# Kernel optimization log

Hardware: AMD Instinct MI355X
Metric: run time of the kernel (lower is better)

## Reference

```python
import jax, jax.numpy as jnp
import numpy as np

N_NODES = 50000
N_EDGES = 800000
IN_FEATS = 64
HIDDEN = 32
HEADS = 8
NEG_SLOPE = 0.2


def gat_conv(x, W, a_l, a_r, b, src, dst, num_nodes):
    """DGL-style GATConv. x:[N,in], W:[in,H,O], a_l/a_r/b:[H,O]. Returns [N,H,O]."""
    feat = jnp.einsum('ni,iho->nho', x, W)              # [N,H,O]
    el = jnp.sum(feat * a_l, axis=-1)                   # [N,H]
    er = jnp.sum(feat * a_r, axis=-1)                   # [N,H]
    e = jax.nn.leaky_relu(el[src] + er[dst], NEG_SLOPE) # [E,H]
    # segment softmax over incoming edges of each dst node
    m = jax.ops.segment_max(e, dst, num_segments=num_nodes)   # [N,H]
    ex = jnp.exp(e - m[dst])                                   # [E,H]
    s = jax.ops.segment_sum(ex, dst, num_segments=num_nodes)   # [N,H]
    alpha = ex / s[dst]                                        # [E,H]
    out = jax.ops.segment_sum(feat[src] * alpha[:, :, None], dst,
                              num_segments=num_nodes)          # [N,H,O]
    return out + b


def setup_inputs() -> dict:
    key = jax.random.key(0)
    ks = jax.random.split(key, 12)
    g1 = 1.0 / np.sqrt(IN_FEATS)
    g2 = 1.0 / np.sqrt(HIDDEN * HEADS)
    return {
        'features': jax.random.normal(ks[0], (N_NODES, IN_FEATS), jnp.float32),
        'src': jax.random.randint(ks[1], (N_EDGES,), 0, N_NODES, jnp.int32),
        'dst': jax.random.randint(ks[2], (N_EDGES,), 0, N_NODES, jnp.int32),
        'edge_types': jax.random.randint(ks[3], (N_EDGES,), 0, 4, jnp.int32),
        'W1': jax.random.normal(ks[4], (IN_FEATS, HEADS, HIDDEN), jnp.float32) * g1,
        'al1': jax.random.normal(ks[5], (HEADS, HIDDEN), jnp.float32) * g1,
        'ar1': jax.random.normal(ks[6], (HEADS, HIDDEN), jnp.float32) * g1,
        'b1': jnp.zeros((HEADS, HIDDEN), jnp.float32),
        'W2': jax.random.normal(ks[7], (HIDDEN * HEADS, 1, 1), jnp.float32) * g2,
        'al2': jax.random.normal(ks[8], (1, 1), jnp.float32) * g2,
        'ar2': jax.random.normal(ks[9], (1, 1), jnp.float32) * g2,
        'b2': jnp.zeros((1, 1), jnp.float32),
    }


def reference(features, src, dst, edge_types, W1, al1, ar1, b1, W2, al2, ar2, b2):
    h = gat_conv(features, W1, al1, ar1, b1, src, dst, N_NODES)  # [N,H,O]
    h = jax.nn.relu(h.reshape(h.shape[0], -1))                   # [N,H*O]
    h = gat_conv(h, W2, al2, ar2, b2, src, dst, N_NODES)         # [N,1,1]
    h = jnp.squeeze(h, axis=1)                                   # [N,1]
    return jax.nn.sigmoid(h)
```

## Files before the change

kernel.cpp:

```cpp
#include <hip/hip_runtime.h>

#define N_NODES 50000
#define N_EDGES 800000
#define FEAT_BLOCKS 3125
#define CAP 64

typedef unsigned int uint32;
typedef unsigned short ushort16;
typedef unsigned char uchar8;
typedef short bf8v __attribute__((ext_vector_type(8)));
typedef float f32x4 __attribute__((ext_vector_type(4)));

__device__ __forceinline__ ushort16 f2bf(float f) {
  uint32 u = __float_as_uint(f);
  u += 0x7fffu + ((u >> 16) & 1u);
  return (ushort16)(u >> 16);
}

__global__ __launch_bounds__(256) void k_init(const float* __restrict__ W1,
    ushort16* __restrict__ w1t, int4* __restrict__ deg4) {
  int b = blockIdx.x, t = threadIdx.x;
  if (b < 64) {
    int col = b * 4 + (t >> 6), k = t & 63;
    w1t[col * 64 + k] = f2bf(W1[k * 256 + col]);
  } else {
    int i = (b - 64) * 256 + t;
    if (i < 12500) deg4[i] = make_int4(0, 0, 0, 0);
  }
}

__global__ __launch_bounds__(256) void k_build_feat(const float* __restrict__ x,
    const ushort16* __restrict__ w1t, const float* __restrict__ al1,
    const float* __restrict__ ar1, uchar8* __restrict__ feat8,
    float* __restrict__ el1, float* __restrict__ er1,
    const int* __restrict__ src, const int* __restrict__ dst,
    int* __restrict__ deg, unsigned short* __restrict__ esrc16) {
  int t = threadIdx.x;
  int q = blockIdx.x / 5, r = blockIdx.x % 5;
  if (r == 4) {
    int e0 = q * 1024 + t;
#pragma unroll
    for (int j = 0; j < 4; ++j) {
      int e = e0 + j * 256;
      if (e < N_EDGES) {
        int d = dst[e];
        int sV = src[e];
        int p = atomicAdd(&deg[d], 1);
        if (p < CAP) esrc16[d * CAP + p] = (unsigned short)sV;
      }
    }
    return;
  }
  int fidx = q * 4 + r;
  if (fidx >= FEAT_BLOCKS) return;
  int w = t >> 6, lane = t & 63;
  int quad = lane >> 4, m = lane & 15;
  int n0 = fidx * 16;
  const float* xr = x + (n0 + m) * 64 + quad * 8;
  float4 xa = *(const float4*)(xr);
  float4 xbv = *(const float4*)(xr + 4);
  float4 xc = *(const float4*)(xr + 32);
  float4 xd = *(const float4*)(xr + 36);
  bf8v a0, a1;
  a0[0] = (short)f2bf(xa.x); a0[1] = (short)f2bf(xa.y);
  a0[2] = (short)f2bf(xa.z); a0[3] = (short)f2bf(xa.w);
  a0[4] = (short)f2bf(xbv.x); a0[5] = (short)f2bf(xbv.y);
  a0[6] = (short)f2bf(xbv.z); a0[7] = (short)f2bf(xbv.w);
  a1[0] = (short)f2bf(xc.x); a1[1] = (short)f2bf(xc.y);
  a1[2] = (short)f2bf(xc.z); a1[3] = (short)f2bf(xc.w);
  a1[4] = (short)f2bf(xd.x); a1[5] = (short)f2bf(xd.y);
  a1[6] = (short)f2bf(xd.z); a1[7] = (short)f2bf(xd.w);
  float pl0[4] = {0.f, 0.f, 0.f, 0.f}, pr0[4] = {0.f, 0.f, 0.f, 0.f};
  float pl1[4] = {0.f, 0.f, 0.f, 0.f}, pr1[4] = {0.f, 0.f, 0.f, 0.f};
#pragma unroll
  for (int nt = 0; nt < 4; ++nt) {
    int colg = w * 64 + nt * 16 + m;
    const bf8v* bw = (const bf8v*)(w1t + colg * 64 + quad * 8);
    bf8v b0 = bw[0];
    bf8v b1 = bw[4];
    f32x4 acc = {0.f, 0.f, 0.f, 0.f};
    acc = __builtin_amdgcn_mfma_f32_16x16x32_bf16(a0, b0, acc, 0, 0, 0);
    acc = __builtin_amdgcn_mfma_f32_16x16x32_bf16(a1, b1, acc, 0, 0, 0);
    float al = al1[colg], ar = ar1[colg];
#pragma unroll
    for (int i = 0; i < 4; ++i) {
      uint32 pb = (uint32)__builtin_amdgcn_cvt_pk_fp8_f32(acc[i], acc[i], 0, 0);
      feat8[(size_t)(n0 + quad * 4 + i) * 256 + colg] = (uchar8)(pb & 0xffu);
      if (nt < 2) { pl0[i] += acc[i] * al; pr0[i] += acc[i] * ar; }
      else        { pl1[i] += acc[i] * al; pr1[i] += acc[i] * ar; }
    }
  }
#pragma unroll
  for (int off = 1; off < 16; off <<= 1) {
#pragma unroll
    for (int i = 0; i < 4; ++i) {
      pl0[i] += __shfl_xor(pl0[i], off, 64);
      pr0[i] += __shfl_xor(pr0[i], off, 64);
      pl1[i] += __shfl_xor(pl1[i], off, 64);
      pr1[i] += __shfl_xor(pr1[i], off, 64);
    }
  }
  if (m == 0) {
#pragma unroll
    for (int i = 0; i < 4; ++i) {
      int n = n0 + quad * 4 + i;
      el1[n * 8 + 2 * w] = pl0[i];
      er1[n * 8 + 2 * w] = pr0[i];
      el1[n * 8 + 2 * w + 1] = pl1[i];
      er1[n * 8 + 2 * w + 1] = pr1[i];
    }
  }
}

#define ACC8F8(u, ex)                                                    \
  {                                                                      \
    auto p0 = __builtin_amdgcn_cvt_pk_f32_fp8((u).x, 0);                 \
    auto p1 = __builtin_amdgcn_cvt_pk_f32_fp8((u).x, 1);                 \
    auto p2 = __builtin_amdgcn_cvt_pk_f32_fp8((u).y, 0);                 \
    auto p3 = __builtin_amdgcn_cvt_pk_f32_fp8((u).y, 1);                 \
    acc[0] += p0[0] * (ex); acc[1] += p0[1] * (ex);                      \
    acc[2] += p1[0] * (ex); acc[3] += p1[1] * (ex);                      \
    acc[4] += p2[0] * (ex); acc[5] += p2[1] * (ex);                      \
    acc[6] += p3[0] * (ex); acc[7] += p3[1] * (ex);                      \
  }

__global__ __launch_bounds__(256) void k_agg1(const int* __restrict__ deg,
    const unsigned short* __restrict__ esrc16, const uint2* __restrict__ featv,
    const float* __restrict__ el1, const float* __restrict__ er1,
    const float* __restrict__ b1, const float* __restrict__ W2,
    float* __restrict__ feat2) {
  int t = threadIdx.x, nl = t >> 5, lt = t & 31;
  int n = blockIdx.x * 8 + nl;
  int h = lt >> 2;
  int begin = n * CAP;
  int d = deg[n]; d = d > CAP ? CAP : d;
  int end = begin + d;
  float er_h = er1[n * 8 + h];
  float acc[8] = {0.f, 0.f, 0.f, 0.f, 0.f, 0.f, 0.f, 0.f};
  float s = 0.f;
  int e = begin;
  for (; e + 8 <= end; e += 8) {
    uint4 sv = *(const uint4*)(esrc16 + e);
    int sn[8] = {(int)(sv.x & 0xffffu), (int)(sv.x >> 16),
                 (int)(sv.y & 0xffffu), (int)(sv.y >> 16),
                 (int)(sv.z & 0xffffu), (int)(sv.z >> 16),
                 (int)(sv.w & 0xffffu), (int)(sv.w >> 16)};
    uint2 u[8];
    float ex[8];
#pragma unroll
    for (int j = 0; j < 8; ++j) u[j] = featv[sn[j] * 32 + lt];
#pragma unroll
    for (int j = 0; j < 8; ++j) {
      float v = el1[sn[j] * 8 + h] + er_h;
      v = v > 0.f ? v : 0.2f * v;
      ex[j] = __expf(v);
      s += ex[j];
    }
#pragma unroll
    for (int j = 0; j < 8; ++j) ACC8F8(u[j], ex[j]);
  }
  for (; e + 4 <= end; e += 4) {
    int sn[4];
    uint2 u[4];
    float ex[4];
#pragma unroll
    for (int j = 0; j < 4; ++j) sn[j] = (int)esrc16[e + j];
#pragma unroll
    for (int j = 0; j < 4; ++j) u[j] = featv[sn[j] * 32 + lt];
#pragma unroll
    for (int j = 0; j < 4; ++j) {
      float v = el1[sn[j] * 8 + h] + er_h;
      v = v > 0.f ? v : 0.2f * v;
      ex[j] = __expf(v);
      s += ex[j];
    }
#pragma unroll
    for (int j = 0; j < 4; ++j) ACC8F8(u[j], ex[j]);
  }
  for (; e < end; ++e) {
    int s0 = (int)esrc16[e];
    uint2 u0 = featv[s0 * 32 + lt];
    float v0 = el1[s0 * 8 + h] + er_h;
    v0 = v0 > 0.f ? v0 : 0.2f * v0;
    float ex0 = __expf(v0);
    s += ex0;
    ACC8F8(u0, ex0);
  }
  float inv = (d > 0) ? 1.f / s : 0.f;
  int o = lt * 8;
  float4 bb0 = *(const float4*)(b1 + o), bb1 = *(const float4*)(b1 + o + 4);
  float4 ww0 = *(const float4*)(W2 + o), ww1 = *(const float4*)(W2 + o + 4);
  float r = fmaxf(acc[0] * inv + bb0.x, 0.f) * ww0.x
          + fmaxf(acc[1] * inv + bb0.y, 0.f) * ww0.y
          + fmaxf(acc[2] * inv + bb0.z, 0.f) * ww0.z
          + fmaxf(acc[3] * inv + bb0.w, 0.f) * ww0.w
          + fmaxf(acc[4] * inv + bb1.x, 0.f) * ww1.x
          + fmaxf(acc[5] * inv + bb1.y, 0.f) * ww1.y
          + fmaxf(acc[6] * inv + bb1.z, 0.f) * ww1.z
          + fmaxf(acc[7] * inv + bb1.w, 0.f) * ww1.w;
  __shared__ float red[256];
  red[t] = r;
  __syncthreads();
  for (int off = 16; off > 0; off >>= 1) {
    if (lt < off) red[t] += red[t + off];
    __syncthreads();
  }
  if (lt == 0) feat2[n] = red[t];
}

__global__ __launch_bounds__(256) void k_layer2(const int* __restrict__ deg,
    const unsigned short* __restrict__ esrc16, const float* __restrict__ feat2,
    const float* __restrict__ al2, const float* __restrict__ ar2,
    const float* __restrict__ b2, float* __restrict__ out) {
  int t = threadIdx.x, g = t >> 4, lt = t & 15;
  int n = blockIdx.x * 16 + g;
  int begin = n * CAP;
  int d = deg[n]; d = d > CAP ? CAP : d;
  int end = begin + d;
  float a2 = al2[0];
  float er_n = feat2[n] * ar2[0];
  float num = 0.f, s = 0.f;
  for (int e = begin + lt; e < end; e += 16) {
    int sN = (int)esrc16[e];
    float f = feat2[sN];
    float v = f * a2 + er_n;
    v = v > 0.f ? v : 0.2f * v;
    float ex = __expf(v);
    num += f * ex;
    s += ex;
  }
#pragma unroll
  for (int off = 8; off > 0; off >>= 1) {
    num += __shfl_down(num, off, 16);
    s += __shfl_down(s, off, 16);
  }
  if (lt == 0) {
    float val = (d > 0) ? num / s : 0.f;
    out[n] = 1.f / (1.f + __expf(-(val + b2[0])));
  }
}

extern "C" void kernel_launch(void* const* d_in, const int* in_sizes, int n_in,
                              void* d_out, int out_size, void* d_ws, size_t ws_size,
                              hipStream_t stream) {
  const float* x   = (const float*)d_in[0];
  const int* src   = (const int*)d_in[1];
  const int* dst   = (const int*)d_in[2];
  const float* W1  = (const float*)d_in[4];
  const float* al1 = (const float*)d_in[5];
  const float* ar1 = (const float*)d_in[6];
  const float* b1  = (const float*)d_in[7];
  const float* W2  = (const float*)d_in[8];
  const float* al2 = (const float*)d_in[9];
  const float* ar2 = (const float*)d_in[10];
  const float* b2  = (const float*)d_in[11];

  float* ws    = (float*)d_ws;
  float* el1   = ws;
  float* er1   = ws + 400000;
  float* feat2 = ws + 800000;
  int* deg     = (int*)ws + 850000;
  unsigned short* esrc16 = (unsigned short*)((int*)ws + 900000);
  ushort16* w1t  = (ushort16*)((int*)ws + 2500000);
  uchar8* feat8  = (uchar8*)((int*)ws + 2508192);

  k_init<<<64 + 49, 256, 0, stream>>>(W1, w1t, (int4*)deg);
  k_build_feat<<<3910, 256, 0, stream>>>(x, w1t, al1, ar1, feat8, el1, er1,
                                         src, dst, deg, esrc16);
  k_agg1<<<N_NODES / 8, 256, 0, stream>>>(deg, esrc16, (const uint2*)feat8,
                                          el1, er1, b1, W2, feat2);
  k_layer2<<<N_NODES / 16, 256, 0, stream>>>(deg, esrc16, feat2, al2, ar2, b2,
                                             (float*)d_out);
}
```

Measured before the change: 173.1 us.

## Fuse all four kernels into one persistent kernel with grid barriers

New measurement: 586.9 us. 239% more time.

```diff
diff --git a/kernel.cpp b/kernel.cpp
--- a/kernel.cpp
+++ b/kernel.cpp
@@ -2,8 +2,12 @@
 
 #define N_NODES 50000
 #define N_EDGES 800000
-#define FEAT_BLOCKS 3125
+#define FEAT_ITEMS 3125
+#define SCAT_ITEMS 782
+#define AGG_ITEMS 6250
+#define L2_ITEMS 3125
 #define CAP 64
+#define NBLK 1024
 
 typedef unsigned int uint32;
 typedef unsigned short ushort16;
@@ -17,99 +21,22 @@
   return (ushort16)(u >> 16);
 }
 
-__global__ __launch_bounds__(256) void k_init(const float* __restrict__ W1,
-    ushort16* __restrict__ w1t, int4* __restrict__ deg4) {
-  int b = blockIdx.x, t = threadIdx.x;
-  if (b < 64) {
-    int col = b * 4 + (t >> 6), k = t & 63;
-    w1t[col * 64 + k] = f2bf(W1[k * 256 + col]);
-  } else {
-    int i = (b - 64) * 256 + t;
-    if (i < 12500) deg4[i] = make_int4(0, 0, 0, 0);
-  }
-}
-
-__global__ __launch_bounds__(256) void k_build_feat(const float* __restrict__ x,
-    const ushort16* __restrict__ w1t, const float* __restrict__ al1,
-    const float* __restrict__ ar1, uchar8* __restrict__ feat8,
-    float* __restrict__ el1, float* __restrict__ er1,
-    const int* __restrict__ src, const int* __restrict__ dst,
-    int* __restrict__ deg, unsigned short* __restrict__ esrc16) {
-  int t = threadIdx.x;
-  int q = blockIdx.x / 5, r = blockIdx.x % 5;
-  if (r == 4) {
-    int e0 = q * 1024 + t;
-#pragma unroll
-    for (int j = 0; j < 4; ++j) {
-      int e = e0 + j * 256;
-      if (e < N_EDGES) {
-        int d = dst[e];
-        int sV = src[e];
-        int p = atomicAdd(&deg[d], 1);
-        if (p < CAP) esrc16[d * CAP + p] = (unsigned short)sV;
-      }
-    }
-    return;
-  }
-  int fidx = q * 4 + r;
-  if (fidx >= FEAT_BLOCKS) return;
-  int w = t >> 6, lane = t & 63;
-  int quad = lane >> 4, m = lane & 15;
-  int n0 = fidx * 16;
-  const float* xr = x + (n0 + m) * 64 + quad * 8;
-  float4 xa = *(const float4*)(xr);
-  float4 xbv = *(const float4*)(xr + 4);
-  float4 xc = *(const float4*)(xr + 32);
-  float4 xd = *(const float4*)(xr + 36);
-  bf8v a0, a1;
-  a0[0] = (short)f2bf(xa.x); a0[1] = (short)f2bf(xa.y);
-  a0[2] = (short)f2bf(xa.z); a0[3] = (short)f2bf(xa.w);
-  a0[4] = (short)f2bf(xbv.x); a0[5] = (short)f2bf(xbv.y);
-  a0[6] = (short)f2bf(xbv.z); a0[7] = (short)f2bf(xbv.w);
-  a1[0] = (short)f2bf(xc.x); a1[1] = (short)f2bf(xc.y);
-  a1[2] = (short)f2bf(xc.z); a1[3] = (short)f2bf(xc.w);
-  a1[4] = (short)f2bf(xd.x); a1[5] = (short)f2bf(xd.y);
-  a1[6] = (short)f2bf(xd.z); a1[7] = (short)f2bf(xd.w);
-  float pl0[4] = {0.f, 0.f, 0.f, 0.f}, pr0[4] = {0.f, 0.f, 0.f, 0.f};
-  float pl1[4] = {0.f, 0.f, 0.f, 0.f}, pr1[4] = {0.f, 0.f, 0.f, 0.f};
-#pragma unroll
-  for (int nt = 0; nt < 4; ++nt) {
-    int colg = w * 64 + nt * 16 + m;
-    const bf8v* bw = (const bf8v*)(w1t + colg * 64 + quad * 8);
-    bf8v b0 = bw[0];
-    bf8v b1 = bw[4];
-    f32x4 acc = {0.f, 0.f, 0.f, 0.f};
-    acc = __builtin_amdgcn_mfma_f32_16x16x32_bf16(a0, b0, acc, 0, 0, 0);
-    acc = __builtin_amdgcn_mfma_f32_16x16x32_bf16(a1, b1, acc, 0, 0, 0);
-    float al = al1[colg], ar = ar1[colg];
-#pragma unroll
-    for (int i = 0; i < 4; ++i) {
-      uint32 pb = (uint32)__builtin_amdgcn_cvt_pk_fp8_f32(acc[i], acc[i], 0, 0);
-      feat8[(size_t)(n0 + quad * 4 + i) * 256 + colg] = (uchar8)(pb & 0xffu);
-      if (nt < 2) { pl0[i] += acc[i] * al; pr0[i] += acc[i] * ar; }
-      else        { pl1[i] += acc[i] * al; pr1[i] += acc[i] * ar; }
-    }
-  }
-#pragma unroll
-  for (int off = 1; off < 16; off <<= 1) {
-#pragma unroll
-    for (int i = 0; i < 4; ++i) {
-      pl0[i] += __shfl_xor(pl0[i], off, 64);
-      pr0[i] += __shfl_xor(pr0[i], off, 64);
-      pl1[i] += __shfl_xor(pl1[i], off, 64);
-      pr1[i] += __shfl_xor(pr1[i], off, 64);
-    }
-  }
-  if (m == 0) {
-#pragma unroll
-    for (int i = 0; i < 4; ++i) {
-      int n = n0 + quad * 4 + i;
-      el1[n * 8 + 2 * w] = pl0[i];
-      er1[n * 8 + 2 * w] = pr0[i];
-      el1[n * 8 + 2 * w + 1] = pl1[i];
-      er1[n * 8 + 2 * w + 1] = pr1[i];
-    }
-  }
+__device__ __forceinline__ void gbar(int* cnt, int* gen) {
+  __syncthreads();
+  if (threadIdx.x == 0) {
+    int g = __hip_atomic_load(gen, __ATOMIC_RELAXED, __HIP_MEMORY_SCOPE_AGENT);
+    __threadfence();
+    int a = __hip_atomic_fetch_add(cnt, 1, __ATOMIC_ACQ_REL, __HIP_MEMORY_SCOPE_AGENT);
+    if (a == NBLK - 1) {
+      __hip_atomic_store(cnt, 0, __ATOMIC_RELAXED, __HIP_MEMORY_SCOPE_AGENT);
+      __hip_atomic_fetch_add(gen, 1, __ATOMIC_RELEASE, __HIP_MEMORY_SCOPE_AGENT);
+    } else {
+      while (__hip_atomic_load(gen, __ATOMIC_RELAXED, __HIP_MEMORY_SCOPE_AGENT) == g)
+        __builtin_amdgcn_s_sleep(1);
+    }
+    __threadfence();
+  }
+  __syncthreads();
 }
 
 #define ACC8F8(u, ex)                                                    \
@@ -124,119 +51,197 @@
     acc[6] += p3[0] * (ex); acc[7] += p3[1] * (ex);                      \
   }
 
-__global__ __launch_bounds__(256) void k_agg1(const int* __restrict__ deg,
-    const unsigned short* __restrict__ esrc16, const uint2* __restrict__ featv,
-    const float* __restrict__ el1, const float* __restrict__ er1,
-    const float* __restrict__ b1, const float* __restrict__ W2,
-    float* __restrict__ feat2) {
-  int t = threadIdx.x, nl = t >> 5, lt = t & 31;
-  int n = blockIdx.x * 8 + nl;
-  int h = lt >> 2;
-  int begin = n * CAP;
-  int d = deg[n]; d = d > CAP ? CAP : d;
-  int end = begin + d;
-  float er_h = er1[n * 8 + h];
-  float acc[8] = {0.f, 0.f, 0.f, 0.f, 0.f, 0.f, 0.f, 0.f};
-  float s = 0.f;
-  int e = begin;
-  for (; e + 8 <= end; e += 8) {
-    uint4 sv = *(const uint4*)(esrc16 + e);
-    int sn[8] = {(int)(sv.x & 0xffffu), (int)(sv.x >> 16),
-                 (int)(sv.y & 0xffffu), (int)(sv.y >> 16),
-                 (int)(sv.z & 0xffffu), (int)(sv.z >> 16),
-                 (int)(sv.w & 0xffffu), (int)(sv.w >> 16)};
-    uint2 u[8];
-    float ex[8];
-#pragma unroll
-    for (int j = 0; j < 8; ++j) u[j] = featv[sn[j] * 32 + lt];
-#pragma unroll
-    for (int j = 0; j < 8; ++j) {
-      float v = el1[sn[j] * 8 + h] + er_h;
+__global__ __launch_bounds__(256, 4) void k_fused(const float* __restrict__ x,
+    const float* __restrict__ W1, const float* __restrict__ al1,
+    const float* __restrict__ ar1, const float* __restrict__ b1,
+    const float* __restrict__ W2, const float* __restrict__ al2,
+    const float* __restrict__ ar2, const float* __restrict__ b2,
+    const int* __restrict__ src, const int* __restrict__ dst,
+    float* __restrict__ el1, float* __restrict__ er1, float* __restrict__ feat2,
+    int* __restrict__ deg, unsigned short* __restrict__ esrc16,
+    ushort16* __restrict__ w1t, uchar8* __restrict__ feat8,
+    int* __restrict__ bar_cnt, int* __restrict__ bar_gen,
+    float* __restrict__ out) {
+  int t = threadIdx.x;
+  __shared__ float red[256];
+
+  for (int item = blockIdx.x; item < 113; item += NBLK) {
+    if (item < 64) {
+      int col = item * 4 + (t >> 6), k = t & 63;
+      w1t[col * 64 + k] = f2bf(W1[k * 256 + col]);
+    } else {
+      int i = (item - 64) * 256 + t;
+      if (i < 12500) ((int4*)deg)[i] = make_int4(0, 0, 0, 0);
+    }
+  }
+  gbar(bar_cnt, bar_gen);
+
+  for (int item = blockIdx.x; item < FEAT_ITEMS + SCAT_ITEMS; item += NBLK) {
+    if (item >= FEAT_ITEMS) {
+      int e0 = (item - FEAT_ITEMS) * 1024 + t;
+#pragma unroll
+      for (int j = 0; j < 4; ++j) {
+        int e = e0 + j * 256;
+        if (e < N_EDGES) {
+          int d = dst[e];
+          int sV = src[e];
+          int p = atomicAdd(&deg[d], 1);
+          if (p < CAP) esrc16[d * CAP + p] = (unsigned short)sV;
+        }
+      }
+      continue;
+    }
+    int w = t >> 6, lane = t & 63;
+    int quad = lane >> 4, m = lane & 15;
+    int n0 = item * 16;
+    const float* xr = x + (n0 + m) * 64 + quad * 8;
+    float4 xa = *(const float4*)(xr);
+    float4 xbv = *(const float4*)(xr + 4);
+    float4 xc = *(const float4*)(xr + 32);
+    float4 xd = *(const float4*)(xr + 36);
+    bf8v a0, a1;
+    a0[0] = (short)f2bf(xa.x); a0[1] = (short)f2bf(xa.y);
+    a0[2] = (short)f2bf(xa.z); a0[3] = (short)f2bf(xa.w);
+    a0[4] = (short)f2bf(xbv.x); a0[5] = (short)f2bf(xbv.y);
+    a0[6] = (short)f2bf(xbv.z); a0[7] = (short)f2bf(xbv.w);
+    a1[0] = (short)f2bf(xc.x); a1[1] = (short)f2bf(xc.y);
+    a1[2] = (short)f2bf(xc.z); a1[3] = (short)f2bf(xc.w);
+    a1[4] = (short)f2bf(xd.x); a1[5] = (short)f2bf(xd.y);
+    a1[6] = (short)f2bf(xd.z); a1[7] = (short)f2bf(xd.w);
+    float pl0[4] = {0.f, 0.f, 0.f, 0.f}, pr0[4] = {0.f, 0.f, 0.f, 0.f};
+    float pl1[4] = {0.f, 0.f, 0.f, 0.f}, pr1[4] = {0.f, 0.f, 0.f, 0.f};
+#pragma unroll
+    for (int nt = 0; nt < 4; ++nt) {
+      int colg = w * 64 + nt * 16 + m;
+      const bf8v* bw = (const bf8v*)(w1t + colg * 64 + quad * 8);
+      bf8v b0 = bw[0];
+      bf8v b1v = bw[4];
+      f32x4 acc = {0.f, 0.f, 0.f, 0.f};
+      acc = __builtin_amdgcn_mfma_f32_16x16x32_bf16(a0, b0, acc, 0, 0, 0);
+      acc = __builtin_amdgcn_mfma_f32_16x16x32_bf16(a1, b1v, acc, 0, 0, 0);
+      float al = al1[colg], ar = ar1[colg];
+#pragma unroll
+      for (int i = 0; i < 4; ++i) {
+        uint32 pb = (uint32)__builtin_amdgcn_cvt_pk_fp8_f32(acc[i], acc[i], 0, 0);
+        feat8[(size_t)(n0 + quad * 4 + i) * 256 + colg] = (uchar8)(pb & 0xffu);
+        if (nt < 2) { pl0[i] += acc[i] * al; pr0[i] += acc[i] * ar; }
+        else        { pl1[i] += acc[i] * al; pr1[i] += acc[i] * ar; }
+      }
+    }
+#pragma unroll
+    for (int off = 1; off < 16; off <<= 1) {
+#pragma unroll
+      for (int i = 0; i < 4; ++i) {
+        pl0[i] += __shfl_xor(pl0[i], off, 64);
+        pr0[i] += __shfl_xor(pr0[i], off, 64);
+        pl1[i] += __shfl_xor(pl1[i], off, 64);
+        pr1[i] += __shfl_xor(pr1[i], off, 64);
+      }
+    }
+    if (m == 0) {
+#pragma unroll
+      for (int i = 0; i < 4; ++i) {
+        int n = n0 + quad * 4 + i;
+        el1[n * 8 + 2 * w] = pl0[i];
+        er1[n * 8 + 2 * w] = pr0[i];
+        el1[n * 8 + 2 * w + 1] = pl1[i];
+        er1[n * 8 + 2 * w + 1] = pr1[i];
+      }
+    }
+  }
+  gbar(bar_cnt, bar_gen);
+
+  for (int item = blockIdx.x; item < AGG_ITEMS; item += NBLK) {
+    int nl = t >> 5, lt = t & 31;
+    int n = item * 8 + nl;
+    int h = lt >> 2;
+    int begin = n * CAP;
+    int d = deg[n]; d = d > CAP ? CAP : d;
+    int end = begin + d;
+    float er_h = er1[n * 8 + h];
+    float acc[8] = {0.f, 0.f, 0.f, 0.f, 0.f, 0.f, 0.f, 0.f};
+    float s = 0.f;
+    const uint2* featv = (const uint2*)feat8;
+    int e = begin;
+    for (; e + 8 <= end; e += 8) {
+      uint4 sv = *(const uint4*)(esrc16 + e);
+      int sn[8] = {(int)(sv.x & 0xffffu), (int)(sv.x >> 16),
+                   (int)(sv.y & 0xffffu), (int)(sv.y >> 16),
+                   (int)(sv.z & 0xffffu), (int)(sv.z >> 16),
+                   (int)(sv.w & 0xffffu), (int)(sv.w >> 16)};
+      uint2 u[8];
+      float ex[8];
+#pragma unroll
+      for (int j = 0; j < 8; ++j) u[j] = featv[sn[j] * 32 + lt];
+#pragma unroll
+      for (int j = 0; j < 8; ++j) {
+        float v = el1[sn[j] * 8 + h] + er_h;
+        v = v > 0.f ? v : 0.2f * v;
+        ex[j] = __expf(v);
+        s += ex[j];
+      }
+#pragma unroll
+      for (int j = 0; j < 8; ++j) ACC8F8(u[j], ex[j]);
+    }
+    for (; e < end; ++e) {
+      int s0 = (int)esrc16[e];
+      uint2 u0 = featv[s0 * 32 + lt];
+      float v0 = el1[s0 * 8 + h] + er_h;
+      v0 = v0 > 0.f ? v0 : 0.2f * v0;
+      float ex0 = __expf(v0);
+      s += ex0;
+      ACC8F8(u0, ex0);
+    }
+    float inv = (d > 0) ? 1.f / s : 0.f;
+    int o = lt * 8;
+    float4 bb0 = *(const float4*)(b1 + o), bb1 = *(const float4*)(b1 + o + 4);
+    float4 ww0 = *(const float4*)(W2 + o), ww1 = *(const float4*)(W2 + o + 4);
+    float r = fmaxf(acc[0] * inv + bb0.x, 0.f) * ww0.x
+            + fmaxf(acc[1] * inv + bb0.y, 0.f) * ww0.y
+            + fmaxf(acc[2] * inv + bb0.z, 0.f) * ww0.z
+            + fmaxf(acc[3] * inv + bb0.w, 0.f) * ww0.w
+            + fmaxf(acc[4] * inv + bb1.x, 0.f) * ww1.x
+            + fmaxf(acc[5] * inv + bb1.y, 0.f) * ww1.y
+            + fmaxf(acc[6] * inv + bb1.z, 0.f) * ww1.z
+            + fmaxf(acc[7] * inv + bb1.w, 0.f) * ww1.w;
+    red[t] = r;
+    __syncthreads();
+    for (int off = 16; off > 0; off >>= 1) {
+      if (lt < off) red[t] += red[t + off];
+      __syncthreads();
+    }
+    if (lt == 0) feat2[n] = red[t];
+    __syncthreads();
+  }
+  gbar(bar_cnt, bar_gen);
+
+  for (int item = blockIdx.x; item < L2_ITEMS; item += NBLK) {
+    int g = t >> 4, lt = t & 15;
+    int n = item * 16 + g;
+    int begin = n * CAP;
+    int d = deg[n]; d = d > CAP ? CAP : d;
+    int end = begin + d;
+    float a2 = al2[0];
+    float er_n = feat2[n] * ar2[0];
+    float num = 0.f, s = 0.f;
+    for (int e = begin + lt; e < end; e += 16) {
+      int sN = (int)esrc16[e];
+      float f = feat2[sN];
+      float v = f * a2 + er_n;
       v = v > 0.f ? v : 0.2f * v;
-      ex[j] = __expf(v);
-      s += ex[j];
-    }
-#pragma unroll
-    for (int j = 0; j < 8; ++j) ACC8F8(u[j], ex[j]);
-  }
-  for (; e + 4 <= end; e += 4) {
-    int sn[4];
-    uint2 u[4];
-    float ex[4];
-#pragma unroll
-    for (int j = 0; j < 4; ++j) sn[j] = (int)esrc16[e + j];
-#pragma unroll
-    for (int j = 0; j < 4; ++j) u[j] = featv[sn[j] * 32 + lt];
-#pragma unroll
-    for (int j = 0; j < 4; ++j) {
-      float v = el1[sn[j] * 8 + h] + er_h;
-      v = v > 0.f ? v : 0.2f * v;
-      ex[j] = __expf(v);
-      s += ex[j];
-    }
-#pragma unroll
-    for (int j = 0; j < 4; ++j) ACC8F8(u[j], ex[j]);
-  }
-  for (; e < end; ++e) {
-    int s0 = (int)esrc16[e];
-    uint2 u0 = featv[s0 * 32 + lt];
-    float v0 = el1[s0 * 8 + h] + er_h;
-    v0 = v0 > 0.f ? v0 : 0.2f * v0;
-    float ex0 = __expf(v0);
-    s += ex0;
-    ACC8F8(u0, ex0);
-  }
-  float inv = (d > 0) ? 1.f / s : 0.f;
-  int o = lt * 8;
-  float4 bb0 = *(const float4*)(b1 + o), bb1 = *(const float4*)(b1 + o + 4);
-  float4 ww0 = *(const float4*)(W2 + o), ww1 = *(const float4*)(W2 + o + 4);
-  float r = fmaxf(acc[0] * inv + bb0.x, 0.f) * ww0.x
-          + fmaxf(acc[1] * inv + bb0.y, 0.f) * ww0.y
-          + fmaxf(acc[2] * inv + bb0.z, 0.f) * ww0.z
-          + fmaxf(acc[3] * inv + bb0.w, 0.f) * ww0.w
-          + fmaxf(acc[4] * inv + bb1.x, 0.f) * ww1.x
-          + fmaxf(acc[5] * inv + bb1.y, 0.f) * ww1.y
-          + fmaxf(acc[6] * inv + bb1.z, 0.f) * ww1.z
-          + fmaxf(acc[7] * inv + bb1.w, 0.f) * ww1.w;
-  __shared__ float red[256];
-  red[t] = r;
-  __syncthreads();
-  for (int off = 16; off > 0; off >>= 1) {
-    if (lt < off) red[t] += red[t + off];
-    __syncthreads();
-  }
-  if (lt == 0) feat2[n] = red[t];
-}
-
-__global__ __launch_bounds__(256) void k_layer2(const int* __restrict__ deg,
-    const unsigned short* __restrict__ esrc16, const float* __restrict__ feat2,
-    const float* __restrict__ al2, const float* __restrict__ ar2,
-    const float* __restrict__ b2, float* __restrict__ out) {
-  int t = threadIdx.x, g = t >> 4, lt = t & 15;
-  int n = blockIdx.x * 16 + g;
-  int begin = n * CAP;
-  int d = deg[n]; d = d > CAP ? CAP : d;
-  int end = begin + d;
-  float a2 = al2[0];
-  float er_n = feat2[n] * ar2[0];
-  float num = 0.f, s = 0.f;
-  for (int e = begin + lt; e < end; e += 16) {
-    int sN = (int)esrc16[e];
-    float f = feat2[sN];
-    float v = f * a2 + er_n;
-    v = v > 0.f ? v : 0.2f * v;
-    float ex = __expf(v);
-    num += f * ex;
-    s += ex;
-  }
-#pragma unroll
-  for (int off = 8; off > 0; off >>= 1) {
-    num += __shfl_down(num, off, 16);
-    s += __shfl_down(s, off, 16);
-  }
-  if (lt == 0) {
-    float val = (d > 0) ? num / s : 0.f;
-    out[n] = 1.f / (1.f + __expf(-(val + b2[0])));
+      float ex = __expf(v);
+      num += f * ex;
+      s += ex;
+    }
+#pragma unroll
+    for (int off = 8; off > 0; off >>= 1) {
+      num += __shfl_down(num, off, 16);
+      s += __shfl_down(s, off, 16);
+    }
+    if (lt == 0) {
+      float val = (d > 0) ? num / s : 0.f;
+      out[n] = 1.f / (1.f + __expf(-(val + b2[0])));
+    }
   }
 }
 
@@ -263,12 +268,11 @@
   unsigned short* esrc16 = (unsigned short*)((int*)ws + 900000);
   ushort16* w1t  = (ushort16*)((int*)ws + 2500000);
   uchar8* feat8  = (uchar8*)((int*)ws + 2508192);
-
-  k_init<<<64 + 49, 256, 0, stream>>>(W1, w1t, (int4*)deg);
-  k_build_feat<<<3910, 256, 0, stream>>>(x, w1t, al1, ar1, feat8, el1, er1,
-                                         src, dst, deg, esrc16);
-  k_agg1<<<N_NODES / 8, 256, 0, stream>>>(deg, esrc16, (const uint2*)feat8,
-                                          el1, er1, b1, W2, feat2);
-  k_layer2<<<N_NODES / 16, 256, 0, stream>>>(deg, esrc16, feat2, al2, ar2, b2,
-                                             (float*)d_out);
-}
+  int* bar       = (int*)ws + 5708192;
+
+  hipMemsetAsync(bar, 0, 2 * sizeof(int), stream);
+
+  k_fused<<<NBLK, 256, 0, stream>>>(x, W1, al1, ar1, b1, W2, al2, ar2, b2,
+                                    src, dst, el1, er1, feat2, deg, esrc16,
+                                    w1t, feat8, bar, bar + 1, (float*)d_out);
+}
```
